# Kernel optimization log

Measured on AMD Instinct MI355X. Metric: run time of the kernel, lower is better.

Reference implementation:

```python
import jax, jax.numpy as jnp
import numpy as np

NUM_EXPERTS = 16
TOP_K = 4
N_GROUP = 4
TOPK_GROUP = 2
SCALING = 2.5


def setup_inputs() -> dict:
    key = jax.random.key(0)
    ks = jax.random.split(key, 9)
    B, S, H, I = 2, 1024, 2048, 1024
    w = lambda k, shape: jax.random.normal(k, shape, jnp.float32) * 0.02
    return {
        "hidden_states": jax.random.normal(ks[0], (B, S, H), jnp.float32),
        "gate_weight": w(ks[1], (NUM_EXPERTS, H)),
        "expert_bias": jnp.zeros((NUM_EXPERTS,), jnp.float32),
        "gate_proj": w(ks[2], (NUM_EXPERTS, I, H)),
        "up_proj": w(ks[3], (NUM_EXPERTS, I, H)),
        "down_proj": w(ks[4], (NUM_EXPERTS, H, I)),
        "shared_gate": w(ks[5], (I, H)),
        "shared_up": w(ks[6], (I, H)),
        "shared_down": w(ks[7], (H, I)),
    }


def _route(x, gate_weight, expert_bias):
    # x: [T, H] -> routing weights [T, K], selected experts [T, K]
    logits = x @ gate_weight.T                              # [T, E]
    scores = jax.nn.sigmoid(logits)
    biased = scores + expert_bias[None, :]                  # bias only for selection
    T = x.shape[0]
    gsz = NUM_EXPERTS // N_GROUP
    grp = biased.reshape(T, N_GROUP, gsz)
    top2, _ = jax.lax.top_k(grp, 2)
    group_scores = top2.sum(-1)                             # [T, G]
    _, gidx = jax.lax.top_k(group_scores, TOPK_GROUP)       # [T, topk_group]
    gmask = jax.nn.one_hot(gidx, N_GROUP, dtype=scores.dtype).sum(1)  # [T, G]
    emask = jnp.repeat(gmask, gsz, axis=1)                  # [T, E]
    masked = jnp.where(emask > 0, biased, -jnp.inf)
    _, sel = jax.lax.top_k(masked, TOP_K)                   # [T, K]
    w = jnp.take_along_axis(scores, sel, axis=1)            # weights from unbiased scores
    w = w / (w.sum(-1, keepdims=True) + 1e-20)              # norm_topk_prob
    return w * SCALING, sel


def _moe(x, w, sel, gate_proj, up_proj, down_proj):
    # combine weight per (token, expert): [T, E]; zero where expert not selected
    cw = (jax.nn.one_hot(sel, NUM_EXPERTS, dtype=x.dtype) * w[..., None]).sum(1)

    def body(acc, inp):
        g, u, d, we = inp                                   # g,u: [I,H]; d: [H,I]; we: [T]
        y = (jax.nn.silu(x @ g.T) * (x @ u.T)) @ d.T        # SwiGLU expert FFN
        return acc + we[:, None] * y, None

    out, _ = jax.lax.scan(body, jnp.zeros_like(x),
                          (gate_proj, up_proj, down_proj, cw.T))
    return out


def reference(hidden_states, gate_weight, expert_bias, gate_proj, up_proj,
              down_proj, shared_gate, shared_up, shared_down):
    B, S, H = hidden_states.shape
    x = hidden_states.reshape(-1, H)                        # [T, H]
    w, sel = _route(x, gate_weight, expert_bias)
    out = _moe(x, w, sel, gate_proj, up_proj, down_proj)
    shared = (jax.nn.silu(x @ shared_gate.T) * (x @ shared_up.T)) @ shared_down.T
    return (out + shared).reshape(B, S, H)
```

## Files before the change

### kernel.cpp

```cpp
#include <hip/hip_runtime.h>
#include <hip/hip_bf16.h>
#include <stdint.h>

#define T_TOK 2048
#define HDIM  2048
#define IDIM  1024
#define NEXP  16
#define SCALING 2.5f

typedef __attribute__((ext_vector_type(8))) short bf16x8;
typedef __attribute__((ext_vector_type(4))) float f32x4;

static __device__ __forceinline__ unsigned short f2bf(float f) {
    uint32_t u = __float_as_uint(f);
    u += 0x7FFF + ((u >> 16) & 1);
    return (unsigned short)(u >> 16);
}

#define GLD_LDS16(g, l) \
    __builtin_amdgcn_global_load_lds((const __attribute__((address_space(1))) uint32_t*)(g), \
                                     (__attribute__((address_space(3))) uint32_t*)(l), 16, 0, 0)

__global__ __launch_bounds__(256) void cvt_k(const float* __restrict__ x,
                                             unsigned short* __restrict__ o) {
    int i = (blockIdx.x * 256 + threadIdx.x) * 8;
    float4 f0 = *(const float4*)(x + i);
    float4 f1 = *(const float4*)(x + i + 4);
    union { unsigned short h[8]; uint4 v; } u;
    u.h[0] = f2bf(f0.x); u.h[1] = f2bf(f0.y); u.h[2] = f2bf(f0.z); u.h[3] = f2bf(f0.w);
    u.h[4] = f2bf(f1.x); u.h[5] = f2bf(f1.y); u.h[6] = f2bf(f1.z); u.h[7] = f2bf(f1.w);
    *(uint4*)(o + i) = u.v;
}

__global__ __launch_bounds__(256) void route_k(const float* __restrict__ x,
                                               const float* __restrict__ gw,
                                               const float* __restrict__ bias,
                                               int* __restrict__ tokl,
                                               float* __restrict__ twl,
                                               int* __restrict__ cnt) {
    __shared__ float slog[NEXP];
    int t = blockIdx.x;
    int tid = threadIdx.x;
    int e = tid >> 4, r = tid & 15;
    const float* xp = x + (size_t)t * HDIM;
    const float* wp = gw + (size_t)e * HDIM;
    float p = 0.f;
    for (int j = r; j < HDIM; j += 16) p += xp[j] * wp[j];
    for (int off = 8; off; off >>= 1) p += __shfl_down(p, off, 16);
    if (r == 0) slog[e] = p;
    __syncthreads();
    if (tid == 0) {
        float sc[NEXP], bi[NEXP];
        for (int i = 0; i < NEXP; i++) {
            sc[i] = 1.f / (1.f + expf(-slog[i]));
            bi[i] = sc[i] + bias[i];
        }
        float gsc[4];
        for (int g = 0; g < 4; g++) {
            float v0 = bi[g*4+0], v1 = bi[g*4+1], v2 = bi[g*4+2], v3 = bi[g*4+3];
            float hi01 = fmaxf(v0, v1), lo01 = fminf(v0, v1);
            float hi23 = fmaxf(v2, v3), lo23 = fminf(v2, v3);
            float top1 = fmaxf(hi01, hi23);
            float sec  = fmaxf(fminf(hi01, hi23), (hi01 >= hi23) ? lo01 : lo23);
            gsc[g] = top1 + sec;
        }
        int g0 = 0; for (int g = 1; g < 4; g++) if (gsc[g] > gsc[g0]) g0 = g;
        int g1 = (g0 == 0) ? 1 : 0;
        for (int g = 0; g < 4; g++) if (g != g0 && gsc[g] > gsc[g1]) g1 = g;
        float mk[NEXP];
        for (int i = 0; i < NEXP; i++) {
            int gg = i >> 2;
            mk[i] = (gg == g0 || gg == g1) ? bi[i] : -INFINITY;
        }
        int sel[4]; float wv[4]; float wsum = 0.f;
        for (int k = 0; k < 4; k++) {
            int bmax = 0; float bv = -INFINITY;
            for (int i = 0; i < NEXP; i++) if (mk[i] > bv) { bv = mk[i]; bmax = i; }
            sel[k] = bmax; mk[bmax] = -INFINITY;
            wv[k] = sc[bmax]; wsum += sc[bmax];
        }
        float scale = SCALING / (wsum + 1e-20f);
        for (int k = 0; k < 4; k++) {
            int ee = sel[k];
            int slot = atomicAdd(&cnt[ee], 1);
            tokl[ee * T_TOK + slot] = t;
            twl[ee * T_TOK + slot] = wv[k] * scale;
        }
    }
}

__global__ __launch_bounds__(256) void gemm1_k(const unsigned short* __restrict__ Xbf,
                                               const float* __restrict__ gate_w,
                                               const float* __restrict__ up_w,
                                               const float* __restrict__ sh_gate,
                                               const float* __restrict__ sh_up,
                                               const int* __restrict__ tokl,
                                               const int* __restrict__ cnt,
                                               unsigned short* __restrict__ act) {
    __shared__ unsigned short lsA[2][128 * 64];
    __shared__ unsigned short lsB[2][128 * 64];
    int b = blockIdx.x;
    int swz = (b & 7) * 544 + (b >> 3);
    int mt = swz & 15, nt = (swz >> 4) & 15, e = swz >> 8;
    int C = (e == NEXP) ? T_TOK : cnt[e];
    int m0 = mt * 128;
    if (m0 >= C) return;
    int tid = threadIdx.x;

    int c8 = tid & 7, rr = tid >> 3;
    int swzc = c8 ^ (rr & 7);
    const char* aA[4];
    for (int i = 0; i < 4; i++) {
        int slot = m0 + i * 32 + rr;
        int sl = (slot < C) ? slot : (C - 1);
        int tk = (e == NEXP) ? sl : tokl[e * T_TOK + sl];
        aA[i] = (const char*)Xbf + ((size_t)tk * HDIM + (size_t)swzc * 8) * 2;
    }
    int bg = tid & 15, br0 = tid >> 4;
    const float* pB[8];
    int wOffB[8];
    for (int p = 0; p < 8; p++) {
        int row = p * 16 + br0;
        int f = nt * 64 + (row >> 1);
        const float* base;
        if (e == NEXP) base = (row & 1) ? sh_up : sh_gate;
        else base = ((row & 1) ? up_w : gate_w) + (size_t)e * IDIM * HDIM;
        pB[p] = base + (size_t)f * HDIM + bg * 4;
        wOffB[p] = row * 128 + (((bg >> 1) ^ (row & 7)) << 4) + ((bg & 1) << 3);
    }

    int lane = tid & 63, wid = tid >> 6;
    int wrow = (wid >> 1) << 6, wcol = (wid & 1) << 6;
    int fr = lane & 15, kg = lane >> 4;

    f32x4 acc[4][4];
#pragma unroll
    for (int m = 0; m < 4; m++)
#pragma unroll
        for (int n = 0; n < 4; n++) acc[m][n] = (f32x4){0.f, 0.f, 0.f, 0.f};

    auto stage = [&](int kt, int bf) {
        size_t kb = (size_t)kt * 128;
#pragma unroll
        for (int i = 0; i < 4; i++)
            GLD_LDS16(aA[i] + kb, (char*)&lsA[bf][0] + i * 4096 + tid * 16);
        size_t kf = (size_t)kt * 64;
        char* lB = (char*)&lsB[bf][0];
#pragma unroll
        for (int p = 0; p < 8; p++) {
            float4 f = *(const float4*)(pB[p] + kf);
            uint64_t v = (uint64_t)f2bf(f.x) | ((uint64_t)f2bf(f.y) << 16)
                       | ((uint64_t)f2bf(f.z) << 32) | ((uint64_t)f2bf(f.w) << 48);
            *(uint64_t*)(lB + wOffB[p]) = v;
        }
    };
    auto compute = [&](int bf) {
        const char* lA = (const char*)&lsA[bf][0];
        const char* lB = (const char*)&lsB[bf][0];
#pragma unroll
        for (int h = 0; h < 2; h++) {
            bf16x8 av[4], bv[4];
#pragma unroll
            for (int m = 0; m < 4; m++)
                av[m] = *(const bf16x8*)(lA + (wrow + m * 16 + fr) * 128 + (((h * 4 + kg) ^ (fr & 7)) << 4));
#pragma unroll
            for (int n = 0; n < 4; n++)
                bv[n] = *(const bf16x8*)(lB + (wcol + n * 16 + fr) * 128 + (((h * 4 + kg) ^ (fr & 7)) << 4));
#pragma unroll
            for (int m = 0; m < 4; m++)
#pragma unroll
                for (int n = 0; n < 4; n++)
                    acc[m][n] = __builtin_amdgcn_mfma_f32_16x16x32_bf16(av[m], bv[n], acc[m][n], 0, 0, 0);
        }
    };

    stage(0, 0);
    __syncthreads();
    int cur = 0;
    for (int kt = 0; kt < 32; ++kt) {
        if (kt + 1 < 32) stage(kt + 1, cur ^ 1);
        compute(cur);
        __syncthreads();
        cur ^= 1;
    }

    unsigned short* actE = act + (size_t)e * T_TOK * IDIM;
#pragma unroll
    for (int m = 0; m < 4; m++)
#pragma unroll
        for (int n = 0; n < 4; n++)
#pragma unroll
            for (int q = 0; q < 4; q++) {
                float v = acc[m][n][q];
                float pu = __shfl_xor(v, 1, 64);
                int row = wrow + m * 16 + kg * 4 + q;
                int slot = m0 + row;
                int col = wcol + n * 16 + fr;
                if (!(lane & 1) && slot < C) {
                    float g = v, u = pu;
                    float a = g / (1.f + __expf(-g)) * u;
                    int j = nt * 64 + (col >> 1);
                    actE[(size_t)slot * IDIM + j] = f2bf(a);
                }
            }
}

__global__ __launch_bounds__(256) void gemm2_k(const unsigned short* __restrict__ act,
                                               const float* __restrict__ down_w,
                                               const float* __restrict__ sh_down,
                                               const int* __restrict__ tokl,
                                               const float* __restrict__ twl,
                                               const int* __restrict__ cnt,
                                               float* __restrict__ out) {
    __shared__ unsigned short lsA[2][128 * 64];
    __shared__ unsigned short lsB[2][128 * 64];
    int b = blockIdx.x;
    int swz = (b & 7) * 544 + (b >> 3);
    int mt = swz & 15, nt = (swz >> 4) & 15, e = swz >> 8;
    int C = (e == NEXP) ? T_TOK : cnt[e];
    int m0 = mt * 128;
    if (m0 >= C) return;
    int nb = nt * 128;
    int tid = threadIdx.x;

    const unsigned short* actE = act + (size_t)e * T_TOK * IDIM;
    int c8 = tid & 7, rr = tid >> 3;
    int swzc = c8 ^ (rr & 7);
    const char* aA[4];
    for (int i = 0; i < 4; i++) {
        int slot = m0 + i * 32 + rr;
        aA[i] = (const char*)actE + ((size_t)slot * IDIM + (size_t)swzc * 8) * 2;
    }
    int bg = tid & 15, br0 = tid >> 4;
    const float* pB[8];
    int wOffB[8];
    const float* dbase = (e == NEXP) ? sh_down : (down_w + (size_t)e * HDIM * IDIM);
    for (int p = 0; p < 8; p++) {
        int row = p * 16 + br0;
        pB[p] = dbase + (size_t)(nb + row) * IDIM + bg * 4;
        wOffB[p] = row * 128 + (((bg >> 1) ^ (row & 7)) << 4) + ((bg & 1) << 3);
    }

    int lane = tid & 63, wid = tid >> 6;
    int wrow = (wid >> 1) << 6, wcol = (wid & 1) << 6;
    int fr = lane & 15, kg = lane >> 4;

    f32x4 acc[4][4];
#pragma unroll
    for (int m = 0; m < 4; m++)
#pragma unroll
        for (int n = 0; n < 4; n++) acc[m][n] = (f32x4){0.f, 0.f, 0.f, 0.f};

    auto stage = [&](int kt, int bf) {
        size_t kb = (size_t)kt * 128;
#pragma unroll
        for (int i = 0; i < 4; i++)
            GLD_LDS16(aA[i] + kb, (char*)&lsA[bf][0] + i * 4096 + tid * 16);
        size_t kf = (size_t)kt * 64;
        char* lB = (char*)&lsB[bf][0];
#pragma unroll
        for (int p = 0; p < 8; p++) {
            float4 f = *(const float4*)(pB[p] + kf);
            uint64_t v = (uint64_t)f2bf(f.x) | ((uint64_t)f2bf(f.y) << 16)
                       | ((uint64_t)f2bf(f.z) << 32) | ((uint64_t)f2bf(f.w) << 48);
            *(uint64_t*)(lB + wOffB[p]) = v;
        }
    };
    auto compute = [&](int bf) {
        const char* lA = (const char*)&lsA[bf][0];
        const char* lB = (const char*)&lsB[bf][0];
#pragma unroll
        for (int h = 0; h < 2; h++) {
            bf16x8 av[4], bv[4];
#pragma unroll
            for (int m = 0; m < 4; m++)
                av[m] = *(const bf16x8*)(lA + (wrow + m * 16 + fr) * 128 + (((h * 4 + kg) ^ (fr & 7)) << 4));
#pragma unroll
            for (int n = 0; n < 4; n++)
                bv[n] = *(const bf16x8*)(lB + (wcol + n * 16 + fr) * 128 + (((h * 4 + kg) ^ (fr & 7)) << 4));
#pragma unroll
            for (int m = 0; m < 4; m++)
#pragma unroll
                for (int n = 0; n < 4; n++)
                    acc[m][n] = __builtin_amdgcn_mfma_f32_16x16x32_bf16(av[m], bv[n], acc[m][n], 0, 0, 0);
        }
    };

    stage(0, 0);
    __syncthreads();
    int cur = 0;
    for (int kt = 0; kt < 16; ++kt) {
        if (kt + 1 < 16) stage(kt + 1, cur ^ 1);
        compute(cur);
        __syncthreads();
        cur ^= 1;
    }

#pragma unroll
    for (int m = 0; m < 4; m++)
#pragma unroll
        for (int q = 0; q < 4; q++) {
            int row = wrow + m * 16 + kg * 4 + q;
            int slot = m0 + row;
            if (slot >= C) continue;
            int tk; float wg;
            if (e == NEXP) { tk = slot; wg = 1.f; }
            else { tk = tokl[e * T_TOK + slot]; wg = twl[e * T_TOK + slot]; }
            float* o = out + (size_t)tk * HDIM + nb + wcol + fr;
#pragma unroll
            for (int n = 0; n < 4; n++)
                atomicAdd(o + n * 16, wg * acc[m][n][q]);
        }
}

extern "C" void kernel_launch(void* const* d_in, const int* in_sizes, int n_in,
                              void* d_out, int out_size, void* d_ws, size_t ws_size,
                              hipStream_t stream) {
    const float* x      = (const float*)d_in[0];
    const float* gw     = (const float*)d_in[1];
    const float* bias   = (const float*)d_in[2];
    const float* gate_w = (const float*)d_in[3];
    const float* up_w   = (const float*)d_in[4];
    const float* down_w = (const float*)d_in[5];
    const float* shg    = (const float*)d_in[6];
    const float* shu    = (const float*)d_in[7];
    const float* shd    = (const float*)d_in[8];
    float* out = (float*)d_out;
    char* ws = (char*)d_ws;

    unsigned short* Xbf  = (unsigned short*)ws;
    unsigned short* act  = (unsigned short*)(ws + 8388608);
    int*            tokl = (int*)(ws + 8388608 + 71303168);
    float*          twl  = (float*)(ws + 8388608 + 71303168 + 131072);
    int*            cnt  = (int*)(ws + 8388608 + 71303168 + 262144);

    hipMemsetAsync(out, 0, (size_t)out_size * 4, stream);
    hipMemsetAsync(cnt, 0, 64, stream);
    cvt_k<<<2048, 256, 0, stream>>>(x, Xbf);
    route_k<<<2048, 256, 0, stream>>>(x, gw, bias, tokl, twl, cnt);
    gemm1_k<<<4352, 256, 0, stream>>>(Xbf, gate_w, up_w, shg, shu, tokl, cnt, act);
    gemm2_k<<<4352, 256, 0, stream>>>(act, down_w, shd, tokl, twl, cnt, out);
}
```

Before: 1.008 ms.

## Pre-convert expert weights to bf16 and load them via async LDS copies

Adds two conversion kernels that turn the fp32 gate/up (interleaved) and down weights into bf16 buffers in the workspace once per call. Both GEMMs then stage their B tiles with the same global-to-LDS 16-byte loads used for A, instead of loading fp32 and converting in registers in every tile. This removes repeated per-tile conversion and halves the bytes each tile fetches, at the cost of an extra full pass over all weights and a larger workspace.

```diff
diff --git a/kernel.cpp b/kernel.cpp
--- a/kernel.cpp
+++ b/kernel.cpp
@@ -30,6 +30,45 @@
     u.h[0] = f2bf(f0.x); u.h[1] = f2bf(f0.y); u.h[2] = f2bf(f0.z); u.h[3] = f2bf(f0.w);
     u.h[4] = f2bf(f1.x); u.h[5] = f2bf(f1.y); u.h[6] = f2bf(f1.z); u.h[7] = f2bf(f1.w);
     *(uint4*)(o + i) = u.v;
+}
+
+__global__ __launch_bounds__(256) void cvt_w1_k(const float* __restrict__ gate_w,
+                                                const float* __restrict__ up_w,
+                                                const float* __restrict__ shg,
+                                                const float* __restrict__ shu,
+                                                unsigned short* __restrict__ wbf1) {
+    size_t flat = ((size_t)blockIdx.x * 256 + threadIdx.x) * 8;
+    int e   = (int)(flat >> 22);
+    int rem = (int)(flat & ((1u << 22) - 1));
+    int row = rem >> 11;
+    int h   = rem & 2047;
+    int f   = row >> 1;
+    const float* src;
+    if (e == NEXP) src = (row & 1) ? shu : shg;
+    else           src = ((row & 1) ? up_w : gate_w) + (size_t)e * (IDIM * HDIM);
+    src += (size_t)f * HDIM + h;
+    float4 f0 = *(const float4*)src;
+    float4 f1 = *(const float4*)(src + 4);
+    union { unsigned short s[8]; uint4 v; } u;
+    u.s[0] = f2bf(f0.x); u.s[1] = f2bf(f0.y); u.s[2] = f2bf(f0.z); u.s[3] = f2bf(f0.w);
+    u.s[4] = f2bf(f1.x); u.s[5] = f2bf(f1.y); u.s[6] = f2bf(f1.z); u.s[7] = f2bf(f1.w);
+    *(uint4*)(wbf1 + flat) = u.v;
+}
+
+__global__ __launch_bounds__(256) void cvt_w2_k(const float* __restrict__ down_w,
+                                                const float* __restrict__ shd,
+                                                unsigned short* __restrict__ wbf2) {
+    size_t flat = ((size_t)blockIdx.x * 256 + threadIdx.x) * 8;
+    int e   = (int)(flat >> 21);
+    int rem = (int)(flat & ((1u << 21) - 1));
+    const float* src = (e == NEXP) ? shd : (down_w + (size_t)e * (HDIM * IDIM));
+    src += rem;
+    float4 f0 = *(const float4*)src;
+    float4 f1 = *(const float4*)(src + 4);
+    union { unsigned short s[8]; uint4 v; } u;
+    u.s[0] = f2bf(f0.x); u.s[1] = f2bf(f0.y); u.s[2] = f2bf(f0.z); u.s[3] = f2bf(f0.w);
+    u.s[4] = f2bf(f1.x); u.s[5] = f2bf(f1.y); u.s[6] = f2bf(f1.z); u.s[7] = f2bf(f1.w);
+    *(uint4*)(wbf2 + flat) = u.v;
 }
 
 __global__ __launch_bounds__(256) void route_k(const float* __restrict__ x,
@@ -90,10 +129,7 @@
 }
 
 __global__ __launch_bounds__(256) void gemm1_k(const unsigned short* __restrict__ Xbf,
-                                               const float* __restrict__ gate_w,
-                                               const float* __restrict__ up_w,
-                                               const float* __restrict__ sh_gate,
-                                               const float* __restrict__ sh_up,
+                                               const unsigned short* __restrict__ wbf1,
                                                const int* __restrict__ tokl,
                                                const int* __restrict__ cnt,
                                                unsigned short* __restrict__ act) {
@@ -110,23 +146,14 @@
     int c8 = tid & 7, rr = tid >> 3;
     int swzc = c8 ^ (rr & 7);
     const char* aA[4];
+    const char* aB[4];
     for (int i = 0; i < 4; i++) {
         int slot = m0 + i * 32 + rr;
         int sl = (slot < C) ? slot : (C - 1);
         int tk = (e == NEXP) ? sl : tokl[e * T_TOK + sl];
         aA[i] = (const char*)Xbf + ((size_t)tk * HDIM + (size_t)swzc * 8) * 2;
-    }
-    int bg = tid & 15, br0 = tid >> 4;
-    const float* pB[8];
-    int wOffB[8];
-    for (int p = 0; p < 8; p++) {
-        int row = p * 16 + br0;
-        int f = nt * 64 + (row >> 1);
-        const float* base;
-        if (e == NEXP) base = (row & 1) ? sh_up : sh_gate;
-        else base = ((row & 1) ? up_w : gate_w) + (size_t)e * IDIM * HDIM;
-        pB[p] = base + (size_t)f * HDIM + bg * 4;
-        wOffB[p] = row * 128 + (((bg >> 1) ^ (row & 7)) << 4) + ((bg & 1) << 3);
+        int brow = nt * 128 + i * 32 + rr;
+        aB[i] = (const char*)wbf1 + (((size_t)e << 22) + (size_t)brow * HDIM + (size_t)swzc * 8) * 2;
     }
 
     int lane = tid & 63, wid = tid >> 6;
@@ -144,15 +171,9 @@
 #pragma unroll
         for (int i = 0; i < 4; i++)
             GLD_LDS16(aA[i] + kb, (char*)&lsA[bf][0] + i * 4096 + tid * 16);
-        size_t kf = (size_t)kt * 64;
-        char* lB = (char*)&lsB[bf][0];
-#pragma unroll
-        for (int p = 0; p < 8; p++) {
-            float4 f = *(const float4*)(pB[p] + kf);
-            uint64_t v = (uint64_t)f2bf(f.x) | ((uint64_t)f2bf(f.y) << 16)
-                       | ((uint64_t)f2bf(f.z) << 32) | ((uint64_t)f2bf(f.w) << 48);
-            *(uint64_t*)(lB + wOffB[p]) = v;
-        }
+#pragma unroll
+        for (int i = 0; i < 4; i++)
+            GLD_LDS16(aB[i] + kb, (char*)&lsB[bf][0] + i * 4096 + tid * 16);
     };
     auto compute = [&](int bf) {
         const char* lA = (const char*)&lsA[bf][0];
@@ -206,8 +227,7 @@
 }
 
 __global__ __launch_bounds__(256) void gemm2_k(const unsigned short* __restrict__ act,
-                                               const float* __restrict__ down_w,
-                                               const float* __restrict__ sh_down,
+                                               const unsigned short* __restrict__ wbf2,
                                                const int* __restrict__ tokl,
                                                const float* __restrict__ twl,
                                                const int* __restrict__ cnt,
@@ -227,18 +247,11 @@
     int c8 = tid & 7, rr = tid >> 3;
     int swzc = c8 ^ (rr & 7);
     const char* aA[4];
+    const char* aB[4];
     for (int i = 0; i < 4; i++) {
         int slot = m0 + i * 32 + rr;
         aA[i] = (const char*)actE + ((size_t)slot * IDIM + (size_t)swzc * 8) * 2;
-    }
-    int bg = tid & 15, br0 = tid >> 4;
-    const float* pB[8];
-    int wOffB[8];
-    const float* dbase = (e == NEXP) ? sh_down : (down_w + (size_t)e * HDIM * IDIM);
-    for (int p = 0; p < 8; p++) {
-        int row = p * 16 + br0;
-        pB[p] = dbase + (size_t)(nb + row) * IDIM + bg * 4;
-        wOffB[p] = row * 128 + (((bg >> 1) ^ (row & 7)) << 4) + ((bg & 1) << 3);
+        aB[i] = (const char*)wbf2 + (((size_t)e << 21) + (size_t)(nb + i * 32 + rr) * IDIM + (size_t)swzc * 8) * 2;
     }
 
     int lane = tid & 63, wid = tid >> 6;
@@ -256,15 +269,9 @@
 #pragma unroll
         for (int i = 0; i < 4; i++)
             GLD_LDS16(aA[i] + kb, (char*)&lsA[bf][0] + i * 4096 + tid * 16);
-        size_t kf = (size_t)kt * 64;
-        char* lB = (char*)&lsB[bf][0];
-#pragma unroll
-        for (int p = 0; p < 8; p++) {
-            float4 f = *(const float4*)(pB[p] + kf);
-            uint64_t v = (uint64_t)f2bf(f.x) | ((uint64_t)f2bf(f.y) << 16)
-                       | ((uint64_t)f2bf(f.z) << 32) | ((uint64_t)f2bf(f.w) << 48);
-            *(uint64_t*)(lB + wOffB[p]) = v;
-        }
+#pragma unroll
+        for (int i = 0; i < 4; i++)
+            GLD_LDS16(aB[i] + kb, (char*)&lsB[bf][0] + i * 4096 + tid * 16);
     };
     auto compute = [&](int bf) {
         const char* lA = (const char*)&lsA[bf][0];
@@ -329,15 +336,19 @@
     char* ws = (char*)d_ws;
 
     unsigned short* Xbf  = (unsigned short*)ws;
-    unsigned short* act  = (unsigned short*)(ws + 8388608);
-    int*            tokl = (int*)(ws + 8388608 + 71303168);
-    float*          twl  = (float*)(ws + 8388608 + 71303168 + 131072);
-    int*            cnt  = (int*)(ws + 8388608 + 71303168 + 262144);
+    unsigned short* act  = (unsigned short*)(ws + 8388608ULL);
+    unsigned short* wbf1 = (unsigned short*)(ws + 79691776ULL);
+    unsigned short* wbf2 = (unsigned short*)(ws + 222298112ULL);
+    int*            tokl = (int*)(ws + 293601280ULL);
+    float*          twl  = (float*)(ws + 293732352ULL);
+    int*            cnt  = (int*)(ws + 293863424ULL);
 
     hipMemsetAsync(out, 0, (size_t)out_size * 4, stream);
     hipMemsetAsync(cnt, 0, 64, stream);
     cvt_k<<<2048, 256, 0, stream>>>(x, Xbf);
+    cvt_w1_k<<<34816, 256, 0, stream>>>(gate_w, up_w, shg, shu, wbf1);
+    cvt_w2_k<<<17408, 256, 0, stream>>>(down_w, shd, wbf2);
     route_k<<<2048, 256, 0, stream>>>(x, gw, bias, tokl, twl, cnt);
-    gemm1_k<<<4352, 256, 0, stream>>>(Xbf, gate_w, up_w, shg, shu, tokl, cnt, act);
-    gemm2_k<<<4352, 256, 0, stream>>>(act, down_w, shd, tokl, twl, cnt, out);
-}
+    gemm1_k<<<4352, 256, 0, stream>>>(Xbf, wbf1, tokl, cnt, act);
+    gemm2_k<<<4352, 256, 0, stream>>>(act, wbf2, tokl, twl, cnt, out);
+}
```

Result: slower. 1.046 ms (+3.8%).
